# Kernel optimization log

Hardware: AMD Instinct MI355X
Metric: run time of the kernel (lower is better)

Reference implementation:

```python
import jax, jax.numpy as jnp
import numpy as np

N_NODES = 100000
N_EDGES = 1600000
IN_DIM, HID, OUT_DIM = 128, 128, 64


def _glorot(key, fan_in, fan_out):
    s = float(np.sqrt(6.0 / (fan_in + fan_out)))
    return jax.random.uniform(key, (fan_in, fan_out), jnp.float32, -s, s)


def setup_inputs() -> dict:
    key = jax.random.key(0)
    ks = jax.random.split(key, 6)
    x = jax.random.normal(ks[0], (N_NODES, IN_DIM), jnp.float32)
    edge_index = jax.random.randint(ks[1], (2, N_EDGES), 0, N_NODES, jnp.int32)
    return {
        "x": x,
        "edge_index": edge_index,
        "W0": _glorot(ks[2], IN_DIM, HID), "b0": jnp.zeros((HID,), jnp.float32),
        "W1": _glorot(ks[3], HID, HID),    "b1": jnp.zeros((HID,), jnp.float32),
        "W2": _glorot(ks[4], HID, OUT_DIM), "b2": jnp.zeros((OUT_DIM,), jnp.float32),
    }


def _gcn_conv(x, src, dst, norm, W, b):
    # x' = D^{-1/2} (A+I) D^{-1/2} X W + b  (PyG GCNConv, add_self_loops=True)
    h = x @ W                       # [N, F_out]
    msg = h[src] * norm[:, None]    # [E+N, F_out] gathered, normalized messages
    out = jax.ops.segment_sum(msg, dst, num_segments=x.shape[0])
    return out + b


def reference(x, edge_index, W0, b0, W1, b1, W2, b2):
    n = x.shape[0]
    loop = jnp.arange(n, dtype=edge_index.dtype)
    src = jnp.concatenate([edge_index[0], loop])  # self-loops appended
    dst = jnp.concatenate([edge_index[1], loop])
    deg = jax.ops.segment_sum(jnp.ones_like(src, jnp.float32), dst, num_segments=n)
    dis = jnp.where(deg > 0, jax.lax.rsqrt(jnp.maximum(deg, 1e-12)), 0.0)
    norm = dis[src] * dis[dst]      # symmetric GCN normalization per edge

    h = jax.nn.relu(_gcn_conv(x, src, dst, norm, W0, b0))
    h = jax.nn.relu(_gcn_conv(h, src, dst, norm, W1, b1))
    h = jax.nn.relu(_gcn_conv(h, src, dst, norm, W2, b2))
    return jax.nn.log_softmax(h, axis=1)
```

## Files before the change

kernel.cpp:

```cpp
#include <hip/hip_runtime.h>

#define NN 100000
#define NE 1600000
#define NBK 782
#define NBLK 256
#define CHUNK ((NE + NBLK - 1) / NBLK)

typedef __bf16 bf16x8 __attribute__((ext_vector_type(8)));
typedef float f32x2 __attribute__((ext_vector_type(2)));
typedef float f32x4 __attribute__((ext_vector_type(4)));

#define ACC8_FP8(vv, mm)                                                              \
  {                                                                                   \
    f32x2 p;                                                                          \
    p = __builtin_amdgcn_cvt_pk_f32_fp8((vv).x, 0); acc[0] += (mm) * p[0]; acc[1] += (mm) * p[1]; \
    p = __builtin_amdgcn_cvt_pk_f32_fp8((vv).x, 1); acc[2] += (mm) * p[0]; acc[3] += (mm) * p[1]; \
    p = __builtin_amdgcn_cvt_pk_f32_fp8((vv).y, 0); acc[4] += (mm) * p[0]; acc[5] += (mm) * p[1]; \
    p = __builtin_amdgcn_cvt_pk_f32_fp8((vv).y, 1); acc[6] += (mm) * p[0]; acc[7] += (mm) * p[1]; \
  }


__global__ __launch_bounds__(256) void kW_prep(const float* __restrict__ W0, const float* __restrict__ W1,
                                               const float* __restrict__ W2, __bf16* __restrict__ Wt) {
  int i = blockIdx.x * 256 + threadIdx.x;
  if (i < 16384) {
    int k = i >> 7, n = i & 127;
    Wt[n * 128 + k] = (__bf16)W0[i];
  } else if (i < 32768) {
    int j = i - 16384;
    int k = j >> 7, n = j & 127;
    Wt[16384 + n * 128 + k] = (__bf16)W1[j];
  } else if (i < 40960) {
    int j = i - 32768;
    int k = j >> 6, n = j & 63;
    Wt[32768 + n * 128 + k] = (__bf16)W2[j];
  }
}


__global__ __launch_bounds__(256) void k1_hist(const int* __restrict__ dst, int* __restrict__ bhist) {
  __shared__ int h[NBK];
  int tid = threadIdx.x, b = blockIdx.x;
  for (int i = tid; i < NBK; i += 256) h[i] = 0;
  __syncthreads();
  int base = b * CHUNK, end = min(base + CHUNK, NE);
  for (int e = base + tid; e < end; e += 256) atomicAdd(&h[dst[e] >> 7], 1);
  __syncthreads();
  for (int i = tid; i < NBK; i += 256) bhist[i * NBLK + b] = h[i];
}

__global__ __launch_bounds__(256) void kA2(const int* __restrict__ bhist, int* __restrict__ btot) {
  int w = threadIdx.x >> 6, lane = threadIdx.x & 63;
  int bin = blockIdx.x * 4 + w;
  if (bin >= NBK) return;
  int4 v = *(const int4*)(bhist + bin * NBLK + lane * 4);
  int s = v.x + v.y + v.z + v.w;
#pragma unroll
  for (int off = 32; off > 0; off >>= 1) s += __shfl_xor(s, off);
  if (lane == 0) btot[bin] = s;
}

__global__ __launch_bounds__(1024) void kB_bscan(const int* __restrict__ btot, int* __restrict__ bptr) {
  __shared__ int s[1024];
  int tid = threadIdx.x;
  int v = (tid < NBK) ? btot[tid] : 0;
  s[tid] = v;
  __syncthreads();
  for (int off = 1; off < 1024; off <<= 1) {
    int t = (tid >= off) ? s[tid - off] : 0;
    __syncthreads();
    s[tid] += t;
    __syncthreads();
  }
  if (tid < NBK) bptr[tid + 1] = s[tid];
  if (tid == 0) bptr[0] = 0;
}

__global__ __launch_bounds__(256) void kC2(const int* __restrict__ bhist, const int* __restrict__ bptr,
                                           int* __restrict__ blockbase) {
  int w = threadIdx.x >> 6, lane = threadIdx.x & 63;
  int bin = blockIdx.x * 4 + w;
  if (bin >= NBK) return;
  int4 v = *(const int4*)(bhist + bin * NBLK + lane * 4);
  int ls = v.x + v.y + v.z + v.w;
  int incl = ls;
#pragma unroll
  for (int off = 1; off < 64; off <<= 1) {
    int t = __shfl_up(incl, off);
    if (lane >= off) incl += t;
  }
  int base = bptr[bin] + incl - ls;
  int4 o;
  o.x = base;
  o.y = base + v.x;
  o.z = base + v.x + v.y;
  o.w = base + v.x + v.y + v.z;
  *(int4*)(blockbase + bin * NBLK + lane * 4) = o;
}

__global__ __launch_bounds__(256) void k3_scatter(const int* __restrict__ src, const int* __restrict__ dst,
                                                  const int* __restrict__ blockbase, int* __restrict__ bucketed) {
  __shared__ int cur[NBK];
  int tid = threadIdx.x, b = blockIdx.x;
  for (int i = tid; i < NBK; i += 256) cur[i] = blockbase[i * NBLK + b];
  __syncthreads();
  int base = b * CHUNK, end = min(base + CHUNK, NE);
  for (int e = base + tid; e < end; e += 256) {
    int d = dst[e];
    int pos = atomicAdd(&cur[d >> 7], 1);
    bucketed[pos] = (src[e] << 7) | (d & 127);
  }
}

__global__ __launch_bounds__(256) void k_degfill(const int* __restrict__ bucketed, const int* __restrict__ bptr,
                                                 int* __restrict__ row_ptr, float* __restrict__ dis,
                                                 int* __restrict__ csr_src) {
  __shared__ int deg[128];
  __shared__ int sc[128];
  __shared__ int cur[128];
  int b = blockIdx.x, tid = threadIdx.x;
  int nb0 = b << 7;
  if (tid < 128) deg[tid] = 0;
  __syncthreads();
  int beg = bptr[b], end = bptr[b + 1];
  for (int e = beg + tid; e < end; e += 256) atomicAdd(&deg[bucketed[e] & 127], 1);
  __syncthreads();
  if (tid < 128) sc[tid] = deg[tid];
  __syncthreads();
  for (int off = 1; off < 128; off <<= 1) {
    int t = (tid >= off && tid < 128) ? sc[tid - off] : 0;
    __syncthreads();
    if (tid < 128) sc[tid] += t;
    __syncthreads();
  }
  if (tid < 128) {
    cur[tid] = beg + sc[tid] - deg[tid];
    if (nb0 + tid < NN) {
      row_ptr[nb0 + tid + 1] = beg + sc[tid];
      dis[nb0 + tid] = rsqrtf((float)(deg[tid] + 1));
      if (b == 0 && tid == 0) row_ptr[0] = 0;
    }
  }
  __syncthreads();
  for (int e = beg + tid; e < end; e += 256) {
    int pk = bucketed[e];
    int pos = atomicAdd(&cur[pk & 127], 1);
    csr_src[pos] = pk >> 7;
  }
}


template <int BN, int MODE, bool OUT8>
__global__ __launch_bounds__(256) void k_gemm(const void* __restrict__ Av, const __bf16* __restrict__ Wt,
                                              const float* __restrict__ bias, const float* __restrict__ dis,
                                              void* __restrict__ outv) {
  constexpr int LDK = 136;
  constexpr int NT = BN / 32;
  __shared__ __bf16 lB[BN * LDK];

  const int tid = threadIdx.x;
  const int rowBase = blockIdx.x * 128;
  const int lane = tid & 63;
  const int wid = tid >> 6;
  const int wm = (wid & 1) * 64;
  const int wn = (wid >> 1) * (BN / 2);
  const int lm = lane & 15;
  const int kg = lane >> 4;

  for (int c = tid; c < 16 * BN; c += 256) {
    int n = c >> 4;
    int koff = (c & 15) * 8;
    bf16x8 w = *(const bf16x8*)(Wt + n * 128 + koff);
    *(bf16x8*)&lB[n * LDK + koff] = w;
  }
  __syncthreads();

  f32x4 acc[4][NT] = {};
  const bool full = (rowBase + 128 <= NN);

#pragma unroll 2
  for (int ks = 0; ks < 128; ks += 32) {
    int k0 = ks + kg * 8;
    bf16x8 af[4];
    if constexpr (MODE == 0) {
      const float* A = (const float*)Av;
#pragma unroll
      for (int tm = 0; tm < 4; ++tm) {
        int gr = rowBase + wm + tm * 16 + lm;
        f32x4 a0 = {}, a1 = {};
        if (full || gr < NN) {
          a0 = *(const f32x4*)(A + (size_t)gr * 128 + k0);
          a1 = *(const f32x4*)(A + (size_t)gr * 128 + k0 + 4);
        }
        af[tm] = bf16x8{(__bf16)a0[0], (__bf16)a0[1], (__bf16)a0[2], (__bf16)a0[3],
                        (__bf16)a1[0], (__bf16)a1[1], (__bf16)a1[2], (__bf16)a1[3]};
      }
    } else {
      const __bf16* A = (const __bf16*)Av;
      f32x4 b0 = *(const f32x4*)(bias + k0);
      f32x4 b1 = *(const f32x4*)(bias + k0 + 4);
#pragma unroll
      for (int tm = 0; tm < 4; ++tm) {
        int gr = rowBase + wm + tm * 16 + lm;
        bf16x8 v = {};
        if (full || gr < NN) v = *(const bf16x8*)(A + (size_t)gr * 128 + k0);
        af[tm] = bf16x8{(__bf16)fmaxf((float)v[0] + b0[0], 0.f), (__bf16)fmaxf((float)v[1] + b0[1], 0.f),
                        (__bf16)fmaxf((float)v[2] + b0[2], 0.f), (__bf16)fmaxf((float)v[3] + b0[3], 0.f),
                        (__bf16)fmaxf((float)v[4] + b1[0], 0.f), (__bf16)fmaxf((float)v[5] + b1[1], 0.f),
                        (__bf16)fmaxf((float)v[6] + b1[2], 0.f), (__bf16)fmaxf((float)v[7] + b1[3], 0.f)};
      }
    }
    bf16x8 bfr[NT];
#pragma unroll
    for (int tn = 0; tn < NT; ++tn)
      bfr[tn] = *(const bf16x8*)&lB[(wn + tn * 16 + lm) * LDK + k0];
#pragma unroll
    for (int tm = 0; tm < 4; ++tm)
#pragma unroll
      for (int tn = 0; tn < NT; ++tn)
        acc[tm][tn] = __builtin_amdgcn_mfma_f32_16x16x32_bf16(af[tm], bfr[tn], acc[tm][tn], 0, 0, 0);
  }

#pragma unroll
  for (int tm = 0; tm < 4; ++tm) {
    int r0 = rowBase + wm + tm * 16 + kg * 4;
#pragma unroll
    for (int tn = 0; tn < NT; ++tn) {
      int c0 = wn + tn * 16 + lm;
#pragma unroll
      for (int r = 0; r < 4; ++r) {
        int gr = r0 + r;
        if (full || gr < NN) {
          float val = acc[tm][tn][r] * dis[gr];
          if constexpr (OUT8) {
            unsigned char* o8 = (unsigned char*)outv;
            unsigned pk = __builtin_amdgcn_cvt_pk_fp8_f32(val, val, 0, 0);
            o8[(size_t)gr * BN + c0] = (unsigned char)(pk & 0xffu);
          } else {
            __bf16* ob = (__bf16*)outv;
            ob[(size_t)gr * BN + c0] = (__bf16)val;
          }
        }
      }
    }
  }
}


__global__ __launch_bounds__(256) void k_agg128(const unsigned char* __restrict__ tmp8, const int* __restrict__ row_ptr,
                                                const int* __restrict__ csr_src, const float* __restrict__ dis,
                                                __bf16* __restrict__ agg) {
  int wid = (blockIdx.x * 256 + threadIdx.x) >> 6;
  int lane = threadIdx.x & 63;
  if (wid >= NN) return;
  int grp = lane >> 4;
  int fl = lane & 15;

  int beg = row_ptr[wid];
  int end = row_ptr[wid + 1];

  float acc[8] = {0.f, 0.f, 0.f, 0.f, 0.f, 0.f, 0.f, 0.f};
  if (grp == 0) {
    uint2 sv = *(const uint2*)(tmp8 + (size_t)wid * 128 + fl * 8);
    ACC8_FP8(sv, 1.f);
  }

  for (int base = beg; base < end; base += 64) {
    int cnt = min(64, end - base);
    int sidx = (base + lane < end) ? csr_src[base + lane] : 0;
    int i = 0;
    while (i < cnt) {
      int rem = cnt - i;
      if (rem > 16) {
        uint2 v[8];
#pragma unroll
        for (int u = 0; u < 8; ++u) {
          int s = __shfl(sidx, (i + u * 4 + grp) & 63);
          v[u] = *(const uint2*)(tmp8 + (size_t)s * 128 + fl * 8);
        }
#pragma unroll
        for (int u = 0; u < 8; ++u) {
          float m = (i + u * 4 + grp < cnt) ? 1.f : 0.f;
          ACC8_FP8(v[u], m);
        }
        i += 32;
      } else {
        uint2 v[4];
#pragma unroll
        for (int u = 0; u < 4; ++u) {
          int s = __shfl(sidx, (i + u * 4 + grp) & 63);
          v[u] = *(const uint2*)(tmp8 + (size_t)s * 128 + fl * 8);
        }
#pragma unroll
        for (int u = 0; u < 4; ++u) {
          float m = (i + u * 4 + grp < cnt) ? 1.f : 0.f;
          ACC8_FP8(v[u], m);
        }
        i += 16;
      }
    }
  }

#pragma unroll
  for (int t = 0; t < 8; ++t) acc[t] += __shfl_xor(acc[t], 16);
#pragma unroll
  for (int t = 0; t < 8; ++t) acc[t] += __shfl_xor(acc[t], 32);

  if (grp == 0) {
    float d = dis[wid];
    bf16x8 o;
#pragma unroll
    for (int t = 0; t < 8; ++t) o[t] = (__bf16)(acc[t] * d);
    *(bf16x8*)&agg[(size_t)wid * 128 + fl * 8] = o;
  }
}


__global__ __launch_bounds__(256) void k_agg64_final(const __bf16* __restrict__ tmp, const int* __restrict__ row_ptr,
                                                     const int* __restrict__ csr_src, const float* __restrict__ dis,
                                                     const float* __restrict__ b2, float* __restrict__ out) {
  int wid = (blockIdx.x * 256 + threadIdx.x) >> 6;
  int lane = threadIdx.x & 63;
  if (wid >= NN) return;
  int grp = lane >> 3;
  int fl = lane & 7;

  int beg = row_ptr[wid];
  int end = row_ptr[wid + 1];

  float acc[8];
  {
    bf16x8 sv = {};
    if (grp == 0) sv = *(const bf16x8*)&tmp[(size_t)wid * 64 + fl * 8];
#pragma unroll
    for (int t = 0; t < 8; ++t) acc[t] = (grp == 0) ? (float)sv[t] : 0.f;
  }

  for (int base = beg; base < end; base += 64) {
    int cnt = min(64, end - base);
    int sidx = (base + lane < end) ? csr_src[base + lane] : 0;
    int i = 0;
    while (i < cnt) {
      int rem = cnt - i;
      if (rem > 32) {
        bf16x8 v[8];
#pragma unroll
        for (int u = 0; u < 8; ++u) {
          int s = __shfl(sidx, (i + u * 8 + grp) & 63);
          v[u] = *(const bf16x8*)&tmp[(size_t)s * 64 + fl * 8];
        }
#pragma unroll
        for (int u = 0; u < 8; ++u) {
          float m = (i + u * 8 + grp < cnt) ? 1.f : 0.f;
#pragma unroll
          for (int t = 0; t < 8; ++t) acc[t] += m * (float)v[u][t];
        }
        i += 64;
      } else if (rem > 16) {
        bf16x8 v[4];
#pragma unroll
        for (int u = 0; u < 4; ++u) {
          int s = __shfl(sidx, (i + u * 8 + grp) & 63);
          v[u] = *(const bf16x8*)&tmp[(size_t)s * 64 + fl * 8];
        }
#pragma unroll
        for (int u = 0; u < 4; ++u) {
          float m = (i + u * 8 + grp < cnt) ? 1.f : 0.f;
#pragma unroll
          for (int t = 0; t < 8; ++t) acc[t] += m * (float)v[u][t];
        }
        i += 32;
      } else {
        bf16x8 v[2];
#pragma unroll
        for (int u = 0; u < 2; ++u) {
          int s = __shfl(sidx, (i + u * 8 + grp) & 63);
          v[u] = *(const bf16x8*)&tmp[(size_t)s * 64 + fl * 8];
        }
#pragma unroll
        for (int u = 0; u < 2; ++u) {
          float m = (i + u * 8 + grp < cnt) ? 1.f : 0.f;
#pragma unroll
          for (int t = 0; t < 8; ++t) acc[t] += m * (float)v[u][t];
        }
        i += 16;
      }
    }
  }

#pragma unroll
  for (int t = 0; t < 8; ++t) acc[t] += __shfl_xor(acc[t], 8);
#pragma unroll
  for (int t = 0; t < 8; ++t) acc[t] += __shfl_xor(acc[t], 16);
#pragma unroll
  for (int t = 0; t < 8; ++t) acc[t] += __shfl_xor(acc[t], 32);

  float d = dis[wid];
  float v[8], lm_ = -1e30f;
#pragma unroll
  for (int t = 0; t < 8; ++t) {
    v[t] = fmaxf(acc[t] * d + b2[fl * 8 + t], 0.f);
    lm_ = fmaxf(lm_, v[t]);
  }
#pragma unroll
  for (int off = 32; off > 0; off >>= 1) lm_ = fmaxf(lm_, __shfl_xor(lm_, off));
  float le = 0.f;
#pragma unroll
  for (int t = 0; t < 8; ++t) le += expf(v[t] - lm_);
#pragma unroll
  for (int off = 32; off > 0; off >>= 1) le += __shfl_xor(le, off);
  float logss = logf(le * 0.125f);
  if (grp == 0) {
    float4 o0 = make_float4(v[0] - lm_ - logss, v[1] - lm_ - logss, v[2] - lm_ - logss, v[3] - lm_ - logss);
    float4 o1 = make_float4(v[4] - lm_ - logss, v[5] - lm_ - logss, v[6] - lm_ - logss, v[7] - lm_ - logss);
    *(float4*)&out[(size_t)wid * 64 + fl * 8] = o0;
    *(float4*)&out[(size_t)wid * 64 + fl * 8 + 4] = o1;
  }
}


extern "C" void kernel_launch(void* const* d_in, const int* in_sizes, int n_in,
                              void* d_out, int out_size, void* d_ws, size_t ws_size,
                              hipStream_t stream) {
  const float* x  = (const float*)d_in[0];
  const int*   ei = (const int*)d_in[1];
  const float* W0 = (const float*)d_in[2];
  const float* b0 = (const float*)d_in[3];
  const float* W1 = (const float*)d_in[4];
  const float* b1 = (const float*)d_in[5];
  const float* W2 = (const float*)d_in[6];
  const float* b2 = (const float*)d_in[7];
  const int* esrc = ei;
  const int* edst = ei + NE;

  char* p = (char*)d_ws;
  auto alloc = [&](size_t bytes) {
    char* q = p;
    p += (bytes + 255) & ~(size_t)255;
    return q;
  };
  float*  dis     = (float*)alloc((size_t)NN * 4);
  int*    row_ptr = (int*)alloc((size_t)(NN + 1) * 4);
  int*    btot    = (int*)alloc(NBK * 4);
  int*    bptr    = (int*)alloc((NBK + 1) * 4);
  __bf16* Wt      = (__bf16*)alloc(40960 * 2);
  int*    csr_src = (int*)alloc((size_t)NE * 4);
  char*   tmp     = (char*)alloc((size_t)NN * 128 * 2);
  unsigned char* tmp8 = (unsigned char*)tmp;
  __bf16* tmp16   = (__bf16*)tmp;
  int*    bucketed  = (int*)tmp;
  int*    bhist     = csr_src;
  int*    blockbase = csr_src + NBLK * NBK;

  kW_prep<<<160, 256, 0, stream>>>(W0, W1, W2, Wt);
  k1_hist<<<NBLK, 256, 0, stream>>>(edst, bhist);
  kA2<<<(NBK + 3) / 4, 256, 0, stream>>>(bhist, btot);
  kB_bscan<<<1, 1024, 0, stream>>>(btot, bptr);
  kC2<<<(NBK + 3) / 4, 256, 0, stream>>>(bhist, bptr, blockbase);
  k3_scatter<<<NBLK, 256, 0, stream>>>(esrc, edst, blockbase, bucketed);
  k_degfill<<<NBK, 256, 0, stream>>>(bucketed, bptr, row_ptr, dis, csr_src);

  int gblocks = (NN + 127) / 128;
  int ablocks = (NN * 64 + 255) / 256;

  k_gemm<128, 0, true><<<gblocks, 256, 0, stream>>>(x, Wt, nullptr, dis, tmp8);
  k_agg128<<<ablocks, 256, 0, stream>>>(tmp8, row_ptr, csr_src, dis, (__bf16*)d_out);

  k_gemm<128, 2, true><<<gblocks, 256, 0, stream>>>(d_out, Wt + 16384, b0, dis, tmp8);
  k_agg128<<<ablocks, 256, 0, stream>>>(tmp8, row_ptr, csr_src, dis, (__bf16*)d_out);

  k_gemm<64, 2, false><<<gblocks, 256, 0, stream>>>(d_out, Wt + 32768, b1, dis, tmp16);
  k_agg64_final<<<ablocks, 256, 0, stream>>>(tmp16, row_ptr, csr_src, dis, b2, (float*)d_out);
}
```

Baseline: 382.0 us.

## Use zero sentinel row to drop per-edge masks and rework final softmax reduction

The gemm kernels now write a zero row at index NN of their output, and the aggregation kernels use NN as the padding source index, so out-of-range gather slots read zeros and the per-edge mask multiply is removed. The final 64-wide aggregation adds an 8-edge tail path, replaces the shuffle-xor butterfly over accumulators with a shared-memory exchange, and computes log-softmax one feature per lane using fast exp/log intrinsics. This aims to cut ALU work and the number of shuffles, at the cost of extra gathers of the sentinel row, an LDS barrier, and slightly less accurate math intrinsics. The early return for out-of-range waves is removed in the final kernel, which depends on NN being a multiple of 4.

```diff
diff --git a/kernel.cpp b/kernel.cpp
--- a/kernel.cpp
+++ b/kernel.cpp
@@ -10,13 +10,13 @@
 typedef float f32x2 __attribute__((ext_vector_type(2)));
 typedef float f32x4 __attribute__((ext_vector_type(4)));
 
-#define ACC8_FP8(vv, mm)                                                              \
+#define ACC8_FP8(vv)                                                                  \
   {                                                                                   \
     f32x2 p;                                                                          \
-    p = __builtin_amdgcn_cvt_pk_f32_fp8((vv).x, 0); acc[0] += (mm) * p[0]; acc[1] += (mm) * p[1]; \
-    p = __builtin_amdgcn_cvt_pk_f32_fp8((vv).x, 1); acc[2] += (mm) * p[0]; acc[3] += (mm) * p[1]; \
-    p = __builtin_amdgcn_cvt_pk_f32_fp8((vv).y, 0); acc[4] += (mm) * p[0]; acc[5] += (mm) * p[1]; \
-    p = __builtin_amdgcn_cvt_pk_f32_fp8((vv).y, 1); acc[6] += (mm) * p[0]; acc[7] += (mm) * p[1]; \
+    p = __builtin_amdgcn_cvt_pk_f32_fp8((vv).x, 0); acc[0] += p[0]; acc[1] += p[1];   \
+    p = __builtin_amdgcn_cvt_pk_f32_fp8((vv).x, 1); acc[2] += p[0]; acc[3] += p[1];   \
+    p = __builtin_amdgcn_cvt_pk_f32_fp8((vv).y, 0); acc[4] += p[0]; acc[5] += p[1];   \
+    p = __builtin_amdgcn_cvt_pk_f32_fp8((vv).y, 1); acc[6] += p[0]; acc[7] += p[1];   \
   }
 
 
@@ -156,6 +156,7 @@
                                               void* __restrict__ outv) {
   constexpr int LDK = 136;
   constexpr int NT = BN / 32;
+  constexpr int ROWB = BN * (OUT8 ? 1 : 2);
   __shared__ __bf16 lB[BN * LDK];
 
   const int tid = threadIdx.x;
@@ -166,6 +167,10 @@
   const int wn = (wid >> 1) * (BN / 2);
   const int lm = lane & 15;
   const int kg = lane >> 4;
+
+  if (blockIdx.x == 0 && tid < ROWB / 16) {
+    ((uint4*)((char*)outv + (size_t)NN * ROWB))[tid] = make_uint4(0, 0, 0, 0);
+  }
 
   for (int c = tid; c < 16 * BN; c += 256) {
     int n = c >> 4;
@@ -262,12 +267,12 @@
   float acc[8] = {0.f, 0.f, 0.f, 0.f, 0.f, 0.f, 0.f, 0.f};
   if (grp == 0) {
     uint2 sv = *(const uint2*)(tmp8 + (size_t)wid * 128 + fl * 8);
-    ACC8_FP8(sv, 1.f);
+    ACC8_FP8(sv);
   }
 
   for (int base = beg; base < end; base += 64) {
     int cnt = min(64, end - base);
-    int sidx = (base + lane < end) ? csr_src[base + lane] : 0;
+    int sidx = (base + lane < end) ? csr_src[base + lane] : NN;
     int i = 0;
     while (i < cnt) {
       int rem = cnt - i;
@@ -279,10 +284,7 @@
           v[u] = *(const uint2*)(tmp8 + (size_t)s * 128 + fl * 8);
         }
 #pragma unroll
-        for (int u = 0; u < 8; ++u) {
-          float m = (i + u * 4 + grp < cnt) ? 1.f : 0.f;
-          ACC8_FP8(v[u], m);
-        }
+        for (int u = 0; u < 8; ++u) ACC8_FP8(v[u]);
         i += 32;
       } else {
         uint2 v[4];
@@ -292,10 +294,7 @@
           v[u] = *(const uint2*)(tmp8 + (size_t)s * 128 + fl * 8);
         }
 #pragma unroll
-        for (int u = 0; u < 4; ++u) {
-          float m = (i + u * 4 + grp < cnt) ? 1.f : 0.f;
-          ACC8_FP8(v[u], m);
-        }
+        for (int u = 0; u < 4; ++u) ACC8_FP8(v[u]);
         i += 16;
       }
     }
@@ -319,9 +318,11 @@
 __global__ __launch_bounds__(256) void k_agg64_final(const __bf16* __restrict__ tmp, const int* __restrict__ row_ptr,
                                                      const int* __restrict__ csr_src, const float* __restrict__ dis,
                                                      const float* __restrict__ b2, float* __restrict__ out) {
-  int wid = (blockIdx.x * 256 + threadIdx.x) >> 6;
-  int lane = threadIdx.x & 63;
-  if (wid >= NN) return;
+  __shared__ float xch[4][8][66];
+  int tid = threadIdx.x;
+  int wv = tid >> 6;
+  int wid = (blockIdx.x * 256 + tid) >> 6;
+  int lane = tid & 63;
   int grp = lane >> 3;
   int fl = lane & 7;
 
@@ -338,7 +339,7 @@
 
   for (int base = beg; base < end; base += 64) {
     int cnt = min(64, end - base);
-    int sidx = (base + lane < end) ? csr_src[base + lane] : 0;
+    int sidx = (base + lane < end) ? csr_src[base + lane] : NN;
     int i = 0;
     while (i < cnt) {
       int rem = cnt - i;
@@ -350,11 +351,9 @@
           v[u] = *(const bf16x8*)&tmp[(size_t)s * 64 + fl * 8];
         }
 #pragma unroll
-        for (int u = 0; u < 8; ++u) {
-          float m = (i + u * 8 + grp < cnt) ? 1.f : 0.f;
-#pragma unroll
-          for (int t = 0; t < 8; ++t) acc[t] += m * (float)v[u][t];
-        }
+        for (int u = 0; u < 8; ++u)
+#pragma unroll
+          for (int t = 0; t < 8; ++t) acc[t] += (float)v[u][t];
         i += 64;
       } else if (rem > 16) {
         bf16x8 v[4];
@@ -364,13 +363,11 @@
           v[u] = *(const bf16x8*)&tmp[(size_t)s * 64 + fl * 8];
         }
 #pragma unroll
-        for (int u = 0; u < 4; ++u) {
-          float m = (i + u * 8 + grp < cnt) ? 1.f : 0.f;
-#pragma unroll
-          for (int t = 0; t < 8; ++t) acc[t] += m * (float)v[u][t];
-        }
+        for (int u = 0; u < 4; ++u)
+#pragma unroll
+          for (int t = 0; t < 8; ++t) acc[t] += (float)v[u][t];
         i += 32;
-      } else {
+      } else if (rem > 8) {
         bf16x8 v[2];
 #pragma unroll
         for (int u = 0; u < 2; ++u) {
@@ -378,44 +375,38 @@
           v[u] = *(const bf16x8*)&tmp[(size_t)s * 64 + fl * 8];
         }
 #pragma unroll
-        for (int u = 0; u < 2; ++u) {
-          float m = (i + u * 8 + grp < cnt) ? 1.f : 0.f;
-#pragma unroll
-          for (int t = 0; t < 8; ++t) acc[t] += m * (float)v[u][t];
-        }
+        for (int u = 0; u < 2; ++u)
+#pragma unroll
+          for (int t = 0; t < 8; ++t) acc[t] += (float)v[u][t];
         i += 16;
+      } else {
+        int s = __shfl(sidx, (i + grp) & 63);
+        bf16x8 v = *(const bf16x8*)&tmp[(size_t)s * 64 + fl * 8];
+#pragma unroll
+        for (int t = 0; t < 8; ++t) acc[t] += (float)v[t];
+        i += 8;
       }
     }
   }
 
-#pragma unroll
-  for (int t = 0; t < 8; ++t) acc[t] += __shfl_xor(acc[t], 8);
-#pragma unroll
-  for (int t = 0; t < 8; ++t) acc[t] += __shfl_xor(acc[t], 16);
-#pragma unroll
-  for (int t = 0; t < 8; ++t) acc[t] += __shfl_xor(acc[t], 32);
-
-  float d = dis[wid];
-  float v[8], lm_ = -1e30f;
-#pragma unroll
-  for (int t = 0; t < 8; ++t) {
-    v[t] = fmaxf(acc[t] * d + b2[fl * 8 + t], 0.f);
-    lm_ = fmaxf(lm_, v[t]);
-  }
-#pragma unroll
-  for (int off = 32; off > 0; off >>= 1) lm_ = fmaxf(lm_, __shfl_xor(lm_, off));
-  float le = 0.f;
-#pragma unroll
-  for (int t = 0; t < 8; ++t) le += expf(v[t] - lm_);
+  *(f32x2*)&xch[wv][grp][fl * 8 + 0] = f32x2{acc[0], acc[1]};
+  *(f32x2*)&xch[wv][grp][fl * 8 + 2] = f32x2{acc[2], acc[3]};
+  *(f32x2*)&xch[wv][grp][fl * 8 + 4] = f32x2{acc[4], acc[5]};
+  *(f32x2*)&xch[wv][grp][fl * 8 + 6] = f32x2{acc[6], acc[7]};
+  __syncthreads();
+  float av = 0.f;
+#pragma unroll
+  for (int g = 0; g < 8; ++g) av += xch[wv][g][lane];
+
+  float v = fmaxf(av * dis[wid] + b2[lane], 0.f);
+  float lm = v;
+#pragma unroll
+  for (int off = 32; off > 0; off >>= 1) lm = fmaxf(lm, __shfl_xor(lm, off));
+  float e = __expf(v - lm);
+  float le = e;
 #pragma unroll
   for (int off = 32; off > 0; off >>= 1) le += __shfl_xor(le, off);
-  float logss = logf(le * 0.125f);
-  if (grp == 0) {
-    float4 o0 = make_float4(v[0] - lm_ - logss, v[1] - lm_ - logss, v[2] - lm_ - logss, v[3] - lm_ - logss);
-    float4 o1 = make_float4(v[4] - lm_ - logss, v[5] - lm_ - logss, v[6] - lm_ - logss, v[7] - lm_ - logss);
-    *(float4*)&out[(size_t)wid * 64 + fl * 8] = o0;
-    *(float4*)&out[(size_t)wid * 64 + fl * 8 + 4] = o1;
-  }
+  out[(size_t)wid * 64 + lane] = v - lm - __logf(le);
 }
 
 
@@ -445,7 +436,7 @@
   int*    bptr    = (int*)alloc((NBK + 1) * 4);
   __bf16* Wt      = (__bf16*)alloc(40960 * 2);
   int*    csr_src = (int*)alloc((size_t)NE * 4);
-  char*   tmp     = (char*)alloc((size_t)NN * 128 * 2);
+  char*   tmp     = (char*)alloc((size_t)(NN + 1) * 128 * 2);
   unsigned char* tmp8 = (unsigned char*)tmp;
   __bf16* tmp16   = (__bf16*)tmp;
   int*    bucketed  = (int*)tmp;
```

Measured after the change: 381.2 us. No clear change (-0.2%).
